# Optimization experiments

Hardware: AMD Instinct MI355X
Metric: run time of the kernel (lower is better)

Reference implementation:

```python
import jax, jax.numpy as jnp
import numpy as np

P = 384   # ssm_size
H = 768   # hidden_dim
K = 4     # conv_kernel
BATCH, LEN = 16, 2048


def setup_inputs() -> dict:
    key = jax.random.key(0)
    ks = jax.random.split(key, 12)
    inputs = jax.random.normal(ks[0], (BATCH, LEN, H), jnp.float32)
    # encoder
    Wl = jax.random.normal(ks[1], (H, H), jnp.float32) / np.sqrt(H)
    bl = jnp.zeros((H,), jnp.float32)
    conv_w = jax.random.normal(ks[2], (H, 1, K), jnp.float32) / np.sqrt(K)  # depthwise
    conv_b = jnp.zeros((H,), jnp.float32)
    # selective heads (zero-init in torch; small random for a non-trivial baseline)
    Wr = jax.random.normal(ks[3], (P, H), jnp.float32) * 0.01
    Wth = jax.random.normal(ks[4], (P, H), jnp.float32) * 0.01
    Winj = jax.random.normal(ks[5], (P, H), jnp.float32) * 0.01
    # ring init: |lambda| in [0.9, 1.0], arg in (0, pi)
    u = jax.random.uniform(ks[6], (P,), jnp.float32)
    mags = jnp.sqrt(u * (1.0 ** 2 - 0.9 ** 2) + 0.9 ** 2)
    r_base = jnp.log(mags / (1.0 - mags))              # logit
    args = jax.random.uniform(ks[7], (P,), jnp.float32, minval=1e-3, maxval=np.pi - 1e-3)
    th_base = jnp.arctanh(args / np.pi)
    dt_base = jax.random.normal(ks[8], (P,), jnp.float32) * 0.5
    inj_logit = jnp.full((P,), 2.0, jnp.float32)
    b_std = 1.0 / np.sqrt(H)
    c_std = 1.0 / np.sqrt(P)
    Bp = jax.random.uniform(ks[9], (P, H, 2), jnp.float32, minval=-b_std, maxval=b_std)
    Cp = jax.random.uniform(ks[10], (H, P, 2), jnp.float32, minval=-c_std, maxval=c_std)
    D = jax.random.normal(ks[11], (H,), jnp.float32)
    return dict(inputs=inputs, Wl=Wl, bl=bl, conv_w=conv_w, conv_b=conv_b,
                Wr=Wr, Wth=Wth, Winj=Winj, r_base=r_base, th_base=th_base,
                dt_base=dt_base, inj_logit=inj_logit, Bp=Bp, Cp=Cp, D=D)


def reference(inputs, Wl, bl, conv_w, conv_b, Wr, Wth, Winj,
              r_base, th_base, dt_base, inj_logit, Bp, Cp, D):
    Bsz, L, Hd = inputs.shape
    k = conv_w.shape[-1]
    # --- encoder: linear -> silu -> causal depthwise conv -> silu ---
    feats = jax.nn.silu(inputs @ Wl.T + bl)                       # (B,L,H)
    fc = jnp.transpose(feats, (0, 2, 1))                          # (B,H,L)
    fc = jax.lax.conv_general_dilated(
        fc, conv_w, window_strides=(1,), padding=[(k - 1, 0)],
        dimension_numbers=('NCH', 'OIH', 'NCH'), feature_group_count=Hd)
    feats = jnp.transpose(jax.nn.silu(fc + conv_b[None, :, None]), (0, 2, 1))  # (B,L,H)
    # --- spectral params ---
    r = jax.nn.sigmoid(r_base + feats @ Wr.T)                     # (B,L,P)
    theta = jnp.pi * jnp.tanh(th_base + feats @ Wth.T)            # (B,L,P)
    dt_floor = 0.02
    raw_dt = jax.nn.sigmoid(dt_base)                              # (P,) per_step_dt=False
    dt = jnp.broadcast_to(dt_floor + (1.0 - dt_floor) * raw_dt, r.shape)
    r2 = jnp.maximum(r * r, 1e-8)
    dtc = jnp.maximum(dt, 1e-6)
    cos_t = jnp.cos(theta)
    # imex1 variant
    A = (r2 - 2.0 * r * cos_t + 1.0) / (dtc * dtc * r2)
    G = (1.0 - r2) / (dtc * r2)
    # --- input projection (complex) + selective injection gate ---
    Bc = Bp[..., 0] + 1j * Bp[..., 1]                             # (P,H) complex64
    Cc = Cp[..., 0] + 1j * Cp[..., 1]                             # (H,P)
    bu = inputs.astype(jnp.complex64) @ Bc.T                      # (B,L,P)
    gate = jax.nn.sigmoid(inj_logit + feats @ Winj.T)
    bu = bu * gate
    # --- D-LinOSS IMEX1 scan over time ---
    A_s = jnp.transpose(A, (1, 0, 2))                             # (L,B,P)
    G_s = jnp.transpose(G, (1, 0, 2))
    dt_s = jnp.transpose(dtc, (1, 0, 2))
    bu_s = jnp.transpose(bu, (1, 0, 2))
    z0 = jnp.zeros((Bsz, A.shape[-1]), jnp.complex64)

    def step(carry, t):
        z, x = carry
        At, Gt, dtt, but = t
        S = 1.0 / (1.0 + dtt * Gt)          # implicit damping factor
        z = S * (z - (dtt * At) * x) + (S * dtt) * but
        x = x + dtt * z
        return (z, x), x

    _, xs = jax.lax.scan(step, (z0, z0), (A_s, G_s, dt_s, bu_s))  # (L,B,P)
    states = jnp.transpose(xs, (1, 0, 2))                         # (B,L,P)
    proj = jnp.real(states @ Cc.T)                                # (B,L,H)
    return proj + inputs * D
```

## Files before the change

kernel.cpp:

```cpp
#include <hip/hip_runtime.h>
#include <math.h>

#define PP 384
#define HH 768
#define KK 4
#define BB 16
#define LL 2048
#define MM (BB*LL)
#define NCH (BB*PP)
#define NC 32
#define CLEN (LL/NC)

typedef __attribute__((ext_vector_type(8))) short bf16x8;
typedef __attribute__((ext_vector_type(4))) float f32x4;

__device__ __forceinline__ float sigmoid_fast(float x) { return 1.0f / (1.0f + __expf(-x)); }

__device__ __forceinline__ float bf2f(unsigned short h) {
    return __uint_as_float(((unsigned int)h) << 16);
}
__device__ __forceinline__ unsigned short f2bf(float x) {
    unsigned int u = __float_as_uint(x);
    u += 0x7fff + ((u >> 16) & 1);
    return (unsigned short)(u >> 16);
}
__device__ __forceinline__ void split_bf(float x, unsigned short& hi, unsigned short& lo) {
    hi = f2bf(x);
    lo = f2bf(x - bf2f(hi));
}

__device__ __forceinline__ void gll16(const void* g, void* l) {
    __builtin_amdgcn_global_load_lds(
        (const __attribute__((address_space(1))) void*)g,
        (__attribute__((address_space(3))) void*)l, 16, 0, 0);
}

__device__ __forceinline__ void xcd_swizzle(int& bx, int& by) {
    const int gx = (int)gridDim.x;
    const int nwg = gx * (int)gridDim.y;
    const int orig = by * gx + bx;
    const int q = nwg >> 3, r = nwg & 7;
    const int xcd = orig & 7, off = orig >> 3;
    const int swz = (xcd < r ? xcd * (q + 1) : r * (q + 1) + (xcd - r) * q) + off;
    bx = swz % gx;
    by = swz / gx;
}

__device__ __forceinline__ void step_coef(float Rp, float Tp, float Ip,
    float rb, float tb, float il, float dt,
    float& c0, float& c1, float& gdt)
{
    const float PIf = 3.14159265358979323846f;
    float r  = sigmoid_fast(rb + Rp);
    float t  = tb + Tp;
    float e2 = __expf(2.0f * fabsf(t));
    float th = PIf * copysignf(1.0f - 2.0f / (e2 + 1.0f), t);
    float ct = __cosf(th);
    float r2 = fmaxf(r * r, 1e-8f);
    float Ac = (r2 - 2.0f * r * ct + 1.0f) / (dt * dt * r2);
    float Gc = (1.0f - r2) / (dt * r2);
    float S  = 1.0f / (1.0f + dt * Gc);
    float gate = sigmoid_fast(il + Ip);
    c0 = S;
    c1 = S * (dt * Ac);
    gdt = S * dt * gate;
}

__global__ __launch_bounds__(256) void repack_kernel(
    const float* __restrict__ Wl, const float* __restrict__ Wr,
    const float* __restrict__ Wth, const float* __restrict__ Winj,
    const float* __restrict__ Bp, const float* __restrict__ Cp,
    unsigned short* __restrict__ wlh, unsigned short* __restrict__ wll,
    unsigned short* __restrict__ wrth_h, unsigned short* __restrict__ wrth_l,
    unsigned short* __restrict__ winj,
    unsigned short* __restrict__ wb, unsigned short* __restrict__ wc)
{
    int i = blockIdx.x * 256 + threadIdx.x;
    const int NB = 768 * 768, NI = 384 * 768;
    if (i < NB) { split_bf(Wl[i], wlh[i], wll[i]); return; }
    i -= NB;
    if (i < NB) {
        int n = i / 768, k = i - n * 768;
        float v = (n < 384) ? Wr[n * 768 + k] : Wth[(n - 384) * 768 + k];
        split_bf(v, wrth_h[i], wrth_l[i]);
        return;
    }
    i -= NB;
    if (i < NI) { winj[i] = f2bf(Winj[i]); return; }
    i -= NI;
    if (i < NB) {
        int n = i / 768, k = i - n * 768;
        wb[i] = f2bf((n < 384) ? Bp[n * 1536 + k * 2] : Bp[(n - 384) * 1536 + k * 2 + 1]);
        return;
    }
    i -= NB;
    if (i < NB) {
        int n = i / 768, k = i - n * 768;
        wc[i] = f2bf((k < 384) ? Cp[n * 768 + k * 2] : -Cp[n * 768 + (k - 384) * 2 + 1]);
    }
}

__global__ __launch_bounds__(256) void split_convert_kernel(
    const float* __restrict__ in, unsigned short* __restrict__ outh,
    unsigned short* __restrict__ outl, int n4)
{
    int i = blockIdx.x * 256 + threadIdx.x;
    if (i >= n4) return;
    float4 a = ((const float4*)in)[i];
    ushort4 h, l;
    split_bf(a.x, h.x, l.x); split_bf(a.y, h.y, l.y);
    split_bf(a.z, h.z, l.z); split_bf(a.w, h.w, l.w);
    ((ushort4*)outh)[i] = h;
    ((ushort4*)outl)[i] = l;
}

template <int SMODE>
__global__ __launch_bounds__(256) void mfma_gemm_split(
    const unsigned short* __restrict__ Ah, const unsigned short* __restrict__ Al,
    const unsigned short* __restrict__ Wh, const unsigned short* __restrict__ Wl,
    float* __restrict__ Cout, int N, const float* __restrict__ bias)
{
    constexpr int K = 768;
    __shared__ unsigned short lsAh[128 * 32];
    __shared__ unsigned short lsAl[128 * 32];
    __shared__ unsigned short lsBh[128 * 32];
    __shared__ unsigned short lsBl[128 * 32];
    const int tid  = threadIdx.x;
    const int wave = tid >> 6, lane = tid & 63;
    const int wm = wave >> 1, wn = wave & 1;
    int bx = blockIdx.x, by = blockIdx.y;
    xcd_swizzle(bx, by);
    const int row0 = by * 128, col0 = bx * 128;

    const int srow = (wave << 4) + (lane >> 2);
    const int scol = (lane & 3) << 3;
    const size_t ga0 = (size_t)(row0 + srow) * K + scol;
    const size_t ga1 = (size_t)(row0 + 64 + srow) * K + scol;
    const size_t gb0 = (size_t)(col0 + srow) * K + scol;
    const size_t gb1 = (size_t)(col0 + 64 + srow) * K + scol;
    const int l0 = srow * 32 + scol;
    const int l1 = (64 + srow) * 32 + scol;

    f32x4 acc[4][4];
#pragma unroll
    for (int i = 0; i < 4; ++i)
#pragma unroll
        for (int j = 0; j < 4; ++j) acc[i][j] = (f32x4){0.f, 0.f, 0.f, 0.f};

    const int rfo = ((lane & 15) * 32) + ((lane >> 4) << 3);

    for (int kt = 0; kt < K; kt += 32) {
        __syncthreads();
        gll16(Ah + ga0 + kt, &lsAh[l0]);
        gll16(Ah + ga1 + kt, &lsAh[l1]);
        gll16(Al + ga0 + kt, &lsAl[l0]);
        gll16(Al + ga1 + kt, &lsAl[l1]);
        gll16(Wh + gb0 + kt, &lsBh[l0]);
        gll16(Wh + gb1 + kt, &lsBh[l1]);
        gll16(Wl + gb0 + kt, &lsBl[l0]);
        gll16(Wl + gb1 + kt, &lsBl[l1]);
        __syncthreads();
        bf16x8 afh[4], afl[4], bfh[4], bfl[4];
#pragma unroll
        for (int i = 0; i < 4; ++i) {
            afh[i] = *(const bf16x8*)&lsAh[(wm * 64 + i * 16) * 32 + rfo];
            afl[i] = *(const bf16x8*)&lsAl[(wm * 64 + i * 16) * 32 + rfo];
        }
#pragma unroll
        for (int j = 0; j < 4; ++j) {
            bfh[j] = *(const bf16x8*)&lsBh[(wn * 64 + j * 16) * 32 + rfo];
            bfl[j] = *(const bf16x8*)&lsBl[(wn * 64 + j * 16) * 32 + rfo];
        }
#pragma unroll
        for (int i = 0; i < 4; ++i)
#pragma unroll
            for (int j = 0; j < 4; ++j) {
                acc[i][j] = __builtin_amdgcn_mfma_f32_16x16x32_bf16(afh[i], bfh[j], acc[i][j], 0, 0, 0);
                acc[i][j] = __builtin_amdgcn_mfma_f32_16x16x32_bf16(afh[i], bfl[j], acc[i][j], 0, 0, 0);
                acc[i][j] = __builtin_amdgcn_mfma_f32_16x16x32_bf16(afl[i], bfh[j], acc[i][j], 0, 0, 0);
            }
    }

    const int rbase = row0 + wm * 64 + ((lane >> 4) << 2);
    const int cbase = col0 + wn * 64 + (lane & 15);
#pragma unroll
    for (int i = 0; i < 4; ++i) {
#pragma unroll
        for (int j = 0; j < 4; ++j) {
            const int cg = cbase + j * 16;
            float bv = (SMODE == 1) ? bias[cg] : 0.f;
#pragma unroll
            for (int q = 0; q < 4; ++q) {
                const int rg = rbase + i * 16 + q;
                const size_t off = (size_t)rg * N + cg;
                float v = acc[i][j][q];
                if (SMODE == 1) {
                    float x = v + bv;
                    Cout[off] = x * sigmoid_fast(x);
                } else {
                    Cout[off] = v;
                }
            }
        }
    }
}

template <int MODE>
__global__ __launch_bounds__(256) void mfma_gemm(
    const unsigned short* __restrict__ A, const unsigned short* __restrict__ W,
    void* __restrict__ Cout, int N,
    const float* __restrict__ resid, const float* __restrict__ Dv)
{
    constexpr int K = 768;
    __shared__ unsigned short lsA[128 * 32];
    __shared__ unsigned short lsB[128 * 32];
    const int tid  = threadIdx.x;
    const int wave = tid >> 6, lane = tid & 63;
    const int wm = wave >> 1, wn = wave & 1;
    int bx = blockIdx.x, by = blockIdx.y;
    xcd_swizzle(bx, by);
    const int row0 = by * 128, col0 = bx * 128;

    const int srow = (wave << 4) + (lane >> 2);
    const int scol = (lane & 3) << 3;
    const size_t ga0 = (size_t)(row0 + srow) * K + scol;
    const size_t ga1 = (size_t)(row0 + 64 + srow) * K + scol;
    const size_t gb0 = (size_t)(col0 + srow) * K + scol;
    const size_t gb1 = (size_t)(col0 + 64 + srow) * K + scol;
    const int l0 = srow * 32 + scol;
    const int l1 = (64 + srow) * 32 + scol;

    f32x4 acc[4][4];
#pragma unroll
    for (int i = 0; i < 4; ++i)
#pragma unroll
        for (int j = 0; j < 4; ++j) acc[i][j] = (f32x4){0.f, 0.f, 0.f, 0.f};

    const int rfo = ((lane & 15) * 32) + ((lane >> 4) << 3);

    for (int kt = 0; kt < K; kt += 32) {
        __syncthreads();
        gll16(A + ga0 + kt, &lsA[l0]);
        gll16(A + ga1 + kt, &lsA[l1]);
        gll16(W + gb0 + kt, &lsB[l0]);
        gll16(W + gb1 + kt, &lsB[l1]);
        __syncthreads();
        bf16x8 af[4], bfg[4];
#pragma unroll
        for (int i = 0; i < 4; ++i)
            af[i] = *(const bf16x8*)&lsA[(wm * 64 + i * 16) * 32 + rfo];
#pragma unroll
        for (int j = 0; j < 4; ++j)
            bfg[j] = *(const bf16x8*)&lsB[(wn * 64 + j * 16) * 32 + rfo];
#pragma unroll
        for (int i = 0; i < 4; ++i)
#pragma unroll
            for (int j = 0; j < 4; ++j)
                acc[i][j] = __builtin_amdgcn_mfma_f32_16x16x32_bf16(af[i], bfg[j], acc[i][j], 0, 0, 0);
    }

    const int rbase = row0 + wm * 64 + ((lane >> 4) << 2);
    const int cbase = col0 + wn * 64 + (lane & 15);
#pragma unroll
    for (int i = 0; i < 4; ++i) {
#pragma unroll
        for (int j = 0; j < 4; ++j) {
            const int cg = cbase + j * 16;
            float dv = (MODE == 2) ? Dv[cg] : 0.f;
#pragma unroll
            for (int q = 0; q < 4; ++q) {
                const int rg = rbase + i * 16 + q;
                const size_t off = (size_t)rg * N + cg;
                float v = acc[i][j][q];
                if (MODE == 2) {
                    ((float*)Cout)[off] = v + resid[off] * dv;
                } else {
                    ((unsigned short*)Cout)[off] = f2bf(v);
                }
            }
        }
    }
}

__global__ __launch_bounds__(256) void conv_silu_kernel(
    const float* __restrict__ x, const float* __restrict__ w,
    const float* __restrict__ cb, unsigned short* __restrict__ yh,
    unsigned short* __restrict__ yl)
{
    int idx = blockIdx.x * 256 + threadIdx.x;
    if (idx >= MM * HH) return;
    int h  = idx % HH;
    int ml = idx / HH;
    int l  = ml % LL;
    float acc = cb[h];
#pragma unroll
    for (int j = 0; j < KK; ++j) {
        int d = (KK - 1) - j;
        if (l - d >= 0) acc = fmaf(x[(size_t)(ml - d) * HH + h], w[h * KK + j], acc);
    }
    float y = acc * sigmoid_fast(acc);
    split_bf(y, yh[idx], yl[idx]);
}

__global__ __launch_bounds__(256) void scan_chunk_kernel(
    const float* __restrict__ heads_rt, const unsigned short* __restrict__ heads_inj,
    const unsigned short* __restrict__ bu,
    const float* __restrict__ r_base, const float* __restrict__ th_base,
    const float* __restrict__ dt_base, const float* __restrict__ inj,
    float4* __restrict__ summA, float4* __restrict__ summB)
{
    int g = blockIdx.x * 256 + threadIdx.x;
    if (g >= NC * NCH) return;
    int t = g % NCH;
    int j = g / NCH;
    int b = t / PP, p = t - b * PP;
    const float rb = r_base[p], tb = th_base[p], il = inj[p];
    const float dt = 0.02f + 0.98f * sigmoid_fast(dt_base[p]);
    float m00 = 1.f, m01 = 0.f, m10 = 0.f, m11 = 1.f;
    float vzR = 0.f, vxR = 0.f, vzI = 0.f, vxI = 0.f;
    const int mbase = b * LL + j * CLEN;
    for (int l = 0; l < CLEN; ++l) {
        const size_t m = (size_t)(mbase + l);
        const float Rp = heads_rt[m * 768 + p];
        const float Tp = heads_rt[m * 768 + 384 + p];
        const float Ip = bf2f(heads_inj[m * 384 + p]);
        const float b0 = bf2f(bu[m * 768 + p]);
        const float b1 = bf2f(bu[m * 768 + 384 + p]);
        float c0, c1, gdt;
        step_coef(Rp, Tp, Ip, rb, tb, il, dt, c0, c1, gdt);
        const float azR = gdt * b0, azI = gdt * b1;
        float nm00 = c0 * m00 - c1 * m10;
        float nm01 = c0 * m01 - c1 * m11;
        m10 = fmaf(dt, nm00, m10);
        m11 = fmaf(dt, nm01, m11);
        m00 = nm00; m01 = nm01;
        float nvzR = c0 * vzR - c1 * vxR + azR;
        vxR = fmaf(dt, nvzR, vxR); vzR = nvzR;
        float nvzI = c0 * vzI - c1 * vxI + azI;
        vxI = fmaf(dt, nvzI, vxI); vzI = nvzI;
    }
    summA[g] = make_float4(m00, m01, m10, m11);
    summB[g] = make_float4(vzR, vxR, vzI, vxI);
}

__global__ __launch_bounds__(256) void scan_mid_kernel(
    const float4* __restrict__ summA, const float4* __restrict__ summB,
    float4* __restrict__ starts)
{
    int t = blockIdx.x * 256 + threadIdx.x;
    if (t >= NCH) return;
    float zR = 0.f, xR = 0.f, zI = 0.f, xI = 0.f;
    for (int j = 0; j < NC; ++j) {
        starts[j * NCH + t] = make_float4(zR, xR, zI, xI);
        float4 Mv = summA[j * NCH + t];
        float4 Vv = summB[j * NCH + t];
        float nzR = Mv.x * zR + Mv.y * xR + Vv.x;
        float nxR = Mv.z * zR + Mv.w * xR + Vv.y;
        float nzI = Mv.x * zI + Mv.y * xI + Vv.z;
        float nxI = Mv.z * zI + Mv.w * xI + Vv.w;
        zR = nzR; xR = nxR; zI = nzI; xI = nxI;
    }
}

__global__ __launch_bounds__(256) void scan_apply_kernel(
    const float* __restrict__ heads_rt, const unsigned short* __restrict__ heads_inj,
    const unsigned short* __restrict__ bu,
    const float* __restrict__ r_base, const float* __restrict__ th_base,
    const float* __restrict__ dt_base, const float* __restrict__ inj,
    const float4* __restrict__ starts, unsigned short* __restrict__ states)
{
    int g = blockIdx.x * 256 + threadIdx.x;
    if (g >= NC * NCH) return;
    int t = g % NCH;
    int j = g / NCH;
    int b = t / PP, p = t - b * PP;
    const float rb = r_base[p], tb = th_base[p], il = inj[p];
    const float dt = 0.02f + 0.98f * sigmoid_fast(dt_base[p]);
    float4 s0 = starts[j * NCH + t];
    float zR = s0.x, xR = s0.y, zI = s0.z, xI = s0.w;
    const int mbase = b * LL + j * CLEN;
    for (int l = 0; l < CLEN; ++l) {
        const size_t m = (size_t)(mbase + l);
        const float Rp = heads_rt[m * 768 + p];
        const float Tp = heads_rt[m * 768 + 384 + p];
        const float Ip = bf2f(heads_inj[m * 384 + p]);
        const float b0 = bf2f(bu[m * 768 + p]);
        const float b1 = bf2f(bu[m * 768 + 384 + p]);
        float c0, c1, gdt;
        step_coef(Rp, Tp, Ip, rb, tb, il, dt, c0, c1, gdt);
        zR = c0 * zR - c1 * xR + gdt * b0;
        xR = fmaf(dt, zR, xR);
        zI = c0 * zI - c1 * xI + gdt * b1;
        xI = fmaf(dt, zI, xI);
        states[m * 768 + p]       = f2bf(xR);
        states[m * 768 + 384 + p] = f2bf(xI);
    }
}

extern "C" void kernel_launch(void* const* d_in, const int* in_sizes, int n_in,
                              void* d_out, int out_size, void* d_ws, size_t ws_size,
                              hipStream_t stream)
{
    const float* inputs  = (const float*)d_in[0];
    const float* Wl      = (const float*)d_in[1];
    const float* bl      = (const float*)d_in[2];
    const float* conv_w  = (const float*)d_in[3];
    const float* conv_b  = (const float*)d_in[4];
    const float* Wr      = (const float*)d_in[5];
    const float* Wth     = (const float*)d_in[6];
    const float* Winj    = (const float*)d_in[7];
    const float* r_base  = (const float*)d_in[8];
    const float* th_base = (const float*)d_in[9];
    const float* dt_base = (const float*)d_in[10];
    const float* inj_l   = (const float*)d_in[11];
    const float* Bp      = (const float*)d_in[12];
    const float* Cp      = (const float*)d_in[13];
    const float* Dv      = (const float*)d_in[14];
    float* out = (float*)d_out;

    const size_t NB = 768 * 768, NI = 384 * 768, NMH = (size_t)MM * 768;
    unsigned short* wlh    = (unsigned short*)d_ws;
    unsigned short* wll    = wlh + NB;
    unsigned short* wrth_h = wll + NB;
    unsigned short* wrth_l = wrth_h + NB;
    unsigned short* winj   = wrth_l + NB;
    unsigned short* wb     = winj + NI;
    unsigned short* wc     = wb + NB;
    unsigned short* inh    = wc + NB;
    unsigned short* inl    = inh + NMH;
    unsigned short* f2h    = inl + NMH;
    unsigned short* f2l    = f2h + NMH;
    unsigned short* hinj   = f2l + NMH;
    float* f1       = (float*)(hinj + (size_t)MM * 384);
    float* heads_rt = f1;
    float4* summA = (float4*)(f1 + NMH);
    float4* summB = summA + (size_t)NC * NCH;
    float4* starts= summB + (size_t)NC * NCH;
    unsigned short* bu = (unsigned short*)d_out;
    unsigned short* states = inl;

    {
        int total = (int)(4 * NB + NI);
        repack_kernel<<<(total + 255) / 256, 256, 0, stream>>>(
            Wl, Wr, Wth, Winj, Bp, Cp, wlh, wll, wrth_h, wrth_l, winj, wb, wc);
        int n4 = (int)(NMH / 4);
        split_convert_kernel<<<(n4 + 255) / 256, 256, 0, stream>>>(inputs, inh, inl, n4);
    }
    mfma_gemm_split<1><<<dim3(768 / 128, MM / 128), 256, 0, stream>>>(
        inh, inl, wlh, wll, f1, 768, bl);
    conv_silu_kernel<<<(MM * HH + 255) / 256, 256, 0, stream>>>(f1, conv_w, conv_b, f2h, f2l);
    mfma_gemm_split<0><<<dim3(768 / 128, MM / 128), 256, 0, stream>>>(
        f2h, f2l, wrth_h, wrth_l, heads_rt, 768, nullptr);
    mfma_gemm<3><<<dim3(384 / 128, MM / 128), 256, 0, stream>>>(
        f2h, winj, (void*)hinj, 384, nullptr, nullptr);
    mfma_gemm<3><<<dim3(768 / 128, MM / 128), 256, 0, stream>>>(
        inh, wb, (void*)bu, 768, nullptr, nullptr);
    scan_chunk_kernel<<<(NC * NCH) / 256, 256, 0, stream>>>(
        heads_rt, hinj, bu, r_base, th_base, dt_base, inj_l, summA, summB);
    scan_mid_kernel<<<(NCH + 255) / 256, 256, 0, stream>>>(summA, summB, starts);
    scan_apply_kernel<<<(NC * NCH) / 256, 256, 0, stream>>>(
        heads_rt, hinj, bu, r_base, th_base, dt_base, inj_l, starts, states);
    mfma_gemm<2><<<dim3(768 / 128, MM / 128), 256, 0, stream>>>(
        states, wc, (void*)out, 768, inputs, Dv);
}
```

Baseline: 720.0 us.

## Fuse GEMMs sharing an A operand, interleave complex layouts, vectorize conv and scan

The encoder GEMM and the bu projection now run as one launch with a wider grid, since both read the same input activations. The heads GEMM and the injection-gate GEMM are merged the same way. Blocks pick split-precision or plain bf16 paths by column range. Weight repacking interleaves real/imag and R/theta columns so the scan kernels use float2/ushort2 loads and stores. The depthwise conv is vectorized by 4 channels. The output GEMM now reads the bf16 high part of the inputs as its D residual instead of fp32, which lowers precision slightly. The goal is fewer launches, better load balance and wider memory accesses.

Result: slower. 872.6 us (+21.2%).

```diff
diff --git a/kernel.cpp b/kernel.cpp
--- a/kernel.cpp
+++ b/kernel.cpp
@@ -81,7 +81,8 @@
     i -= NB;
     if (i < NB) {
         int n = i / 768, k = i - n * 768;
-        float v = (n < 384) ? Wr[n * 768 + k] : Wth[(n - 384) * 768 + k];
+        int p = n >> 1;
+        float v = (n & 1) ? Wth[p * 768 + k] : Wr[p * 768 + k];
         split_bf(v, wrth_h[i], wrth_l[i]);
         return;
     }
@@ -90,13 +91,12 @@
     i -= NI;
     if (i < NB) {
         int n = i / 768, k = i - n * 768;
-        wb[i] = f2bf((n < 384) ? Bp[n * 1536 + k * 2] : Bp[(n - 384) * 1536 + k * 2 + 1]);
+        wb[i] = f2bf(Bp[(size_t)(n >> 1) * 1536 + k * 2 + (n & 1)]);
         return;
     }
     i -= NB;
     if (i < NB) {
-        int n = i / 768, k = i - n * 768;
-        wc[i] = f2bf((k < 384) ? Cp[n * 768 + k * 2] : -Cp[n * 768 + (k - 384) * 2 + 1]);
+        wc[i] = f2bf((i & 1) ? -Cp[i] : Cp[i]);
     }
 }
 
@@ -114,13 +114,17 @@
     ((ushort4*)outl)[i] = l;
 }
 
-template <int SMODE>
-__global__ __launch_bounds__(256) void mfma_gemm_split(
+template <int KIND>
+__global__ __launch_bounds__(256) void mfma_gemm_fused(
     const unsigned short* __restrict__ Ah, const unsigned short* __restrict__ Al,
-    const unsigned short* __restrict__ Wh, const unsigned short* __restrict__ Wl,
-    float* __restrict__ Cout, int N, const float* __restrict__ bias)
+    const unsigned short* __restrict__ Wsh, const unsigned short* __restrict__ Wsl,
+    const unsigned short* __restrict__ Wp,
+    float* __restrict__ outS, unsigned short* __restrict__ outP,
+    const float* __restrict__ bias)
 {
     constexpr int K = 768;
+    constexpr int NSPLIT = 768;
+    constexpr int STRIDE_P = (KIND == 0) ? 768 : 384;
     __shared__ unsigned short lsAh[128 * 32];
     __shared__ unsigned short lsAl[128 * 32];
     __shared__ unsigned short lsBh[128 * 32];
@@ -131,15 +135,18 @@
     int bx = blockIdx.x, by = blockIdx.y;
     xcd_swizzle(bx, by);
     const int row0 = by * 128, col0 = bx * 128;
+    const bool is_split = (col0 < NSPLIT);
+    const int bcol0 = is_split ? col0 : col0 - NSPLIT;
 
     const int srow = (wave << 4) + (lane >> 2);
     const int scol = (lane & 3) << 3;
     const size_t ga0 = (size_t)(row0 + srow) * K + scol;
     const size_t ga1 = (size_t)(row0 + 64 + srow) * K + scol;
-    const size_t gb0 = (size_t)(col0 + srow) * K + scol;
-    const size_t gb1 = (size_t)(col0 + 64 + srow) * K + scol;
+    const size_t gb0 = (size_t)(bcol0 + srow) * K + scol;
+    const size_t gb1 = (size_t)(bcol0 + 64 + srow) * K + scol;
     const int l0 = srow * 32 + scol;
     const int l1 = (64 + srow) * 32 + scol;
+    const unsigned short* Bh_src = is_split ? Wsh : Wp;
 
     f32x4 acc[4][4];
 #pragma unroll
@@ -153,32 +160,45 @@
         __syncthreads();
         gll16(Ah + ga0 + kt, &lsAh[l0]);
         gll16(Ah + ga1 + kt, &lsAh[l1]);
-        gll16(Al + ga0 + kt, &lsAl[l0]);
-        gll16(Al + ga1 + kt, &lsAl[l1]);
-        gll16(Wh + gb0 + kt, &lsBh[l0]);
-        gll16(Wh + gb1 + kt, &lsBh[l1]);
-        gll16(Wl + gb0 + kt, &lsBl[l0]);
-        gll16(Wl + gb1 + kt, &lsBl[l1]);
+        gll16(Bh_src + gb0 + kt, &lsBh[l0]);
+        gll16(Bh_src + gb1 + kt, &lsBh[l1]);
+        if (is_split) {
+            gll16(Al + ga0 + kt, &lsAl[l0]);
+            gll16(Al + ga1 + kt, &lsAl[l1]);
+            gll16(Wsl + gb0 + kt, &lsBl[l0]);
+            gll16(Wsl + gb1 + kt, &lsBl[l1]);
+        }
         __syncthreads();
-        bf16x8 afh[4], afl[4], bfh[4], bfl[4];
-#pragma unroll
-        for (int i = 0; i < 4; ++i) {
+        bf16x8 afh[4], bfh[4];
+#pragma unroll
+        for (int i = 0; i < 4; ++i)
             afh[i] = *(const bf16x8*)&lsAh[(wm * 64 + i * 16) * 32 + rfo];
-            afl[i] = *(const bf16x8*)&lsAl[(wm * 64 + i * 16) * 32 + rfo];
+#pragma unroll
+        for (int j = 0; j < 4; ++j)
+            bfh[j] = *(const bf16x8*)&lsBh[(wn * 64 + j * 16) * 32 + rfo];
+        if (is_split) {
+            bf16x8 afl[4], bfl[4];
+#pragma unroll
+            for (int i = 0; i < 4; ++i)
+                afl[i] = *(const bf16x8*)&lsAl[(wm * 64 + i * 16) * 32 + rfo];
+#pragma unroll
+            for (int j = 0; j < 4; ++j)
+                bfl[j] = *(const bf16x8*)&lsBl[(wn * 64 + j * 16) * 32 + rfo];
+#pragma unroll
+            for (int i = 0; i < 4; ++i)
+#pragma unroll
+                for (int j = 0; j < 4; ++j) {
+                    acc[i][j] = __builtin_amdgcn_mfma_f32_16x16x32_bf16(afh[i], bfh[j], acc[i][j], 0, 0, 0);
+                    acc[i][j] = __builtin_amdgcn_mfma_f32_16x16x32_bf16(afh[i], bfl[j], acc[i][j], 0, 0, 0);
+                    acc[i][j] = __builtin_amdgcn_mfma_f32_16x16x32_bf16(afl[i], bfh[j], acc[i][j], 0, 0, 0);
+                }
+        } else {
+#pragma unroll
+            for (int i = 0; i < 4; ++i)
+#pragma unroll
+                for (int j = 0; j < 4; ++j)
+                    acc[i][j] = __builtin_amdgcn_mfma_f32_16x16x32_bf16(afh[i], bfh[j], acc[i][j], 0, 0, 0);
         }
-#pragma unroll
-        for (int j = 0; j < 4; ++j) {
-            bfh[j] = *(const bf16x8*)&lsBh[(wn * 64 + j * 16) * 32 + rfo];
-            bfl[j] = *(const bf16x8*)&lsBl[(wn * 64 + j * 16) * 32 + rfo];
-        }
-#pragma unroll
-        for (int i = 0; i < 4; ++i)
-#pragma unroll
-            for (int j = 0; j < 4; ++j) {
-                acc[i][j] = __builtin_amdgcn_mfma_f32_16x16x32_bf16(afh[i], bfh[j], acc[i][j], 0, 0, 0);
-                acc[i][j] = __builtin_amdgcn_mfma_f32_16x16x32_bf16(afh[i], bfl[j], acc[i][j], 0, 0, 0);
-                acc[i][j] = __builtin_amdgcn_mfma_f32_16x16x32_bf16(afl[i], bfh[j], acc[i][j], 0, 0, 0);
-            }
     }
 
     const int rbase = row0 + wm * 64 + ((lane >> 4) << 2);
@@ -188,28 +208,32 @@
 #pragma unroll
         for (int j = 0; j < 4; ++j) {
             const int cg = cbase + j * 16;
-            float bv = (SMODE == 1) ? bias[cg] : 0.f;
+            float bv = (KIND == 0 && bias) ? bias[cg < NSPLIT ? cg : 0] : 0.f;
 #pragma unroll
             for (int q = 0; q < 4; ++q) {
                 const int rg = rbase + i * 16 + q;
-                const size_t off = (size_t)rg * N + cg;
                 float v = acc[i][j][q];
-                if (SMODE == 1) {
-                    float x = v + bv;
-                    Cout[off] = x * sigmoid_fast(x);
+                if (is_split) {
+                    const size_t off = (size_t)rg * 768 + cg;
+                    if (KIND == 0) {
+                        float x = v + bv;
+                        outS[off] = x * sigmoid_fast(x);
+                    } else {
+                        outS[off] = v;
+                    }
                 } else {
-                    Cout[off] = v;
+                    const size_t off = (size_t)rg * STRIDE_P + (cg - NSPLIT);
+                    outP[off] = f2bf(v);
                 }
             }
         }
     }
 }
 
-template <int MODE>
-__global__ __launch_bounds__(256) void mfma_gemm(
+__global__ __launch_bounds__(256) void mfma_gemm_out(
     const unsigned short* __restrict__ A, const unsigned short* __restrict__ W,
-    void* __restrict__ Cout, int N,
-    const float* __restrict__ resid, const float* __restrict__ Dv)
+    float* __restrict__ Cout, int N,
+    const unsigned short* __restrict__ resid, const float* __restrict__ Dv)
 {
     constexpr int K = 768;
     __shared__ unsigned short lsA[128 * 32];
@@ -266,17 +290,12 @@
 #pragma unroll
         for (int j = 0; j < 4; ++j) {
             const int cg = cbase + j * 16;
-            float dv = (MODE == 2) ? Dv[cg] : 0.f;
+            const float dv = Dv[cg];
 #pragma unroll
             for (int q = 0; q < 4; ++q) {
                 const int rg = rbase + i * 16 + q;
                 const size_t off = (size_t)rg * N + cg;
-                float v = acc[i][j][q];
-                if (MODE == 2) {
-                    ((float*)Cout)[off] = v + resid[off] * dv;
-                } else {
-                    ((unsigned short*)Cout)[off] = f2bf(v);
-                }
+                Cout[off] = acc[i][j][q] + bf2f(resid[off]) * dv;
             }
         }
     }
@@ -287,19 +306,33 @@
     const float* __restrict__ cb, unsigned short* __restrict__ yh,
     unsigned short* __restrict__ yl)
 {
-    int idx = blockIdx.x * 256 + threadIdx.x;
-    if (idx >= MM * HH) return;
-    int h  = idx % HH;
-    int ml = idx / HH;
+    int i4 = blockIdx.x * 256 + threadIdx.x;
+    if (i4 >= MM * HH / 4) return;
+    const int HQ = HH / 4;
+    int h4 = (i4 % HQ) * 4;
+    int ml = i4 / HQ;
     int l  = ml % LL;
-    float acc = cb[h];
+    float a0 = cb[h4], a1 = cb[h4 + 1], a2 = cb[h4 + 2], a3 = cb[h4 + 3];
 #pragma unroll
     for (int j = 0; j < KK; ++j) {
         int d = (KK - 1) - j;
-        if (l - d >= 0) acc = fmaf(x[(size_t)(ml - d) * HH + h], w[h * KK + j], acc);
-    }
-    float y = acc * sigmoid_fast(acc);
-    split_bf(y, yh[idx], yl[idx]);
+        if (l - d >= 0) {
+            float4 xv = *(const float4*)(x + (size_t)(ml - d) * HH + h4);
+            a0 = fmaf(xv.x, w[(h4 + 0) * KK + j], a0);
+            a1 = fmaf(xv.y, w[(h4 + 1) * KK + j], a1);
+            a2 = fmaf(xv.z, w[(h4 + 2) * KK + j], a2);
+            a3 = fmaf(xv.w, w[(h4 + 3) * KK + j], a3);
+        }
+    }
+    float y0 = a0 * sigmoid_fast(a0);
+    float y1 = a1 * sigmoid_fast(a1);
+    float y2 = a2 * sigmoid_fast(a2);
+    float y3 = a3 * sigmoid_fast(a3);
+    ushort4 vh, vl;
+    split_bf(y0, vh.x, vl.x); split_bf(y1, vh.y, vl.y);
+    split_bf(y2, vh.z, vl.z); split_bf(y3, vh.w, vl.w);
+    *(ushort4*)(yh + (size_t)i4 * 4) = vh;
+    *(ushort4*)(yl + (size_t)i4 * 4) = vl;
 }
 
 __global__ __launch_bounds__(256) void scan_chunk_kernel(
@@ -321,13 +354,12 @@
     const int mbase = b * LL + j * CLEN;
     for (int l = 0; l < CLEN; ++l) {
         const size_t m = (size_t)(mbase + l);
-        const float Rp = heads_rt[m * 768 + p];
-        const float Tp = heads_rt[m * 768 + 384 + p];
+        const float2 rt = *(const float2*)(heads_rt + m * 768 + 2 * p);
         const float Ip = bf2f(heads_inj[m * 384 + p]);
-        const float b0 = bf2f(bu[m * 768 + p]);
-        const float b1 = bf2f(bu[m * 768 + 384 + p]);
+        const ushort2 bv = *(const ushort2*)(bu + m * 768 + 2 * p);
+        const float b0 = bf2f(bv.x), b1 = bf2f(bv.y);
         float c0, c1, gdt;
-        step_coef(Rp, Tp, Ip, rb, tb, il, dt, c0, c1, gdt);
+        step_coef(rt.x, rt.y, Ip, rb, tb, il, dt, c0, c1, gdt);
         const float azR = gdt * b0, azI = gdt * b1;
         float nm00 = c0 * m00 - c1 * m10;
         float nm01 = c0 * m01 - c1 * m11;
@@ -381,19 +413,20 @@
     const int mbase = b * LL + j * CLEN;
     for (int l = 0; l < CLEN; ++l) {
         const size_t m = (size_t)(mbase + l);
-        const float Rp = heads_rt[m * 768 + p];
-        const float Tp = heads_rt[m * 768 + 384 + p];
+        const float2 rt = *(const float2*)(heads_rt + m * 768 + 2 * p);
         const float Ip = bf2f(heads_inj[m * 384 + p]);
-        const float b0 = bf2f(bu[m * 768 + p]);
-        const float b1 = bf2f(bu[m * 768 + 384 + p]);
+        const ushort2 bv = *(const ushort2*)(bu + m * 768 + 2 * p);
+        const float b0 = bf2f(bv.x), b1 = bf2f(bv.y);
         float c0, c1, gdt;
-        step_coef(Rp, Tp, Ip, rb, tb, il, dt, c0, c1, gdt);
+        step_coef(rt.x, rt.y, Ip, rb, tb, il, dt, c0, c1, gdt);
         zR = c0 * zR - c1 * xR + gdt * b0;
         xR = fmaf(dt, zR, xR);
         zI = c0 * zI - c1 * xI + gdt * b1;
         xI = fmaf(dt, zI, xI);
-        states[m * 768 + p]       = f2bf(xR);
-        states[m * 768 + 384 + p] = f2bf(xI);
+        ushort2 sv;
+        sv.x = f2bf(xR);
+        sv.y = f2bf(xI);
+        *(ushort2*)(states + m * 768 + 2 * p) = sv;
     }
 }
 
@@ -446,20 +479,16 @@
         int n4 = (int)(NMH / 4);
         split_convert_kernel<<<(n4 + 255) / 256, 256, 0, stream>>>(inputs, inh, inl, n4);
     }
-    mfma_gemm_split<1><<<dim3(768 / 128, MM / 128), 256, 0, stream>>>(
-        inh, inl, wlh, wll, f1, 768, bl);
-    conv_silu_kernel<<<(MM * HH + 255) / 256, 256, 0, stream>>>(f1, conv_w, conv_b, f2h, f2l);
-    mfma_gemm_split<0><<<dim3(768 / 128, MM / 128), 256, 0, stream>>>(
-        f2h, f2l, wrth_h, wrth_l, heads_rt, 768, nullptr);
-    mfma_gemm<3><<<dim3(384 / 128, MM / 128), 256, 0, stream>>>(
-        f2h, winj, (void*)hinj, 384, nullptr, nullptr);
-    mfma_gemm<3><<<dim3(768 / 128, MM / 128), 256, 0, stream>>>(
-        inh, wb, (void*)bu, 768, nullptr, nullptr);
+    mfma_gemm_fused<0><<<dim3(12, MM / 128), 256, 0, stream>>>(
+        inh, inl, wlh, wll, wb, f1, bu, bl);
+    conv_silu_kernel<<<(MM * HH / 4 + 255) / 256, 256, 0, stream>>>(f1, conv_w, conv_b, f2h, f2l);
+    mfma_gemm_fused<1><<<dim3(9, MM / 128), 256, 0, stream>>>(
+        f2h, f2l, wrth_h, wrth_l, winj, heads_rt, hinj, nullptr);
     scan_chunk_kernel<<<(NC * NCH) / 256, 256, 0, stream>>>(
         heads_rt, hinj, bu, r_base, th_base, dt_base, inj_l, summA, summB);
     scan_mid_kernel<<<(NCH + 255) / 256, 256, 0, stream>>>(summA, summB, starts);
     scan_apply_kernel<<<(NC * NCH) / 256, 256, 0, stream>>>(
         heads_rt, hinj, bu, r_base, th_base, dt_base, inj_l, starts, states);
-    mfma_gemm<2><<<dim3(768 / 128, MM / 128), 256, 0, stream>>>(
-        states, wc, (void*)out, 768, inputs, Dv);
-}
+    mfma_gemm_out<<<dim3(6, MM / 128), 256, 0, stream>>>(
+        states, wc, out, 768, inh, Dv);
+}
```

## Interleave real/imag weight columns, vectorize conv and scan accesses, use bf16 residual

Applied to the files above, without the earlier changes.

Repacks the Wr/Wth, B and C weights so real and imaginary (or R and theta) columns sit next to each other. The scan kernels can then load each pair with one float2 or ushort2 access and store states as a pair. The conv+silu kernel is vectorized to process four channels per thread with float4 loads and ushort4 stores. The final GEMM now reads the residual from the bf16-high split of the inputs instead of the fp32 inputs, which cuts traffic but reduces the precision of the D*inputs term.

After: 773.0 us. +7.4%, slower.

```diff
diff --git a/kernel.cpp b/kernel.cpp
--- a/kernel.cpp
+++ b/kernel.cpp
@@ -81,7 +81,8 @@
     i -= NB;
     if (i < NB) {
         int n = i / 768, k = i - n * 768;
-        float v = (n < 384) ? Wr[n * 768 + k] : Wth[(n - 384) * 768 + k];
+        int p = n >> 1;
+        float v = (n & 1) ? Wth[p * 768 + k] : Wr[p * 768 + k];
         split_bf(v, wrth_h[i], wrth_l[i]);
         return;
     }
@@ -90,13 +91,12 @@
     i -= NI;
     if (i < NB) {
         int n = i / 768, k = i - n * 768;
-        wb[i] = f2bf((n < 384) ? Bp[n * 1536 + k * 2] : Bp[(n - 384) * 1536 + k * 2 + 1]);
+        wb[i] = f2bf(Bp[(size_t)(n >> 1) * 1536 + k * 2 + (n & 1)]);
         return;
     }
     i -= NB;
     if (i < NB) {
-        int n = i / 768, k = i - n * 768;
-        wc[i] = f2bf((k < 384) ? Cp[n * 768 + k * 2] : -Cp[n * 768 + (k - 384) * 2 + 1]);
+        wc[i] = f2bf((i & 1) ? -Cp[i] : Cp[i]);
     }
 }
 
@@ -209,7 +209,7 @@
 __global__ __launch_bounds__(256) void mfma_gemm(
     const unsigned short* __restrict__ A, const unsigned short* __restrict__ W,
     void* __restrict__ Cout, int N,
-    const float* __restrict__ resid, const float* __restrict__ Dv)
+    const unsigned short* __restrict__ resid, const float* __restrict__ Dv)
 {
     constexpr int K = 768;
     __shared__ unsigned short lsA[128 * 32];
@@ -266,14 +266,14 @@
 #pragma unroll
         for (int j = 0; j < 4; ++j) {
             const int cg = cbase + j * 16;
-            float dv = (MODE == 2) ? Dv[cg] : 0.f;
+            const float dv = (MODE == 2) ? Dv[cg] : 0.f;
 #pragma unroll
             for (int q = 0; q < 4; ++q) {
                 const int rg = rbase + i * 16 + q;
                 const size_t off = (size_t)rg * N + cg;
                 float v = acc[i][j][q];
                 if (MODE == 2) {
-                    ((float*)Cout)[off] = v + resid[off] * dv;
+                    ((float*)Cout)[off] = v + bf2f(resid[off]) * dv;
                 } else {
                     ((unsigned short*)Cout)[off] = f2bf(v);
                 }
@@ -287,19 +287,33 @@
     const float* __restrict__ cb, unsigned short* __restrict__ yh,
     unsigned short* __restrict__ yl)
 {
-    int idx = blockIdx.x * 256 + threadIdx.x;
-    if (idx >= MM * HH) return;
-    int h  = idx % HH;
-    int ml = idx / HH;
+    int i4 = blockIdx.x * 256 + threadIdx.x;
+    if (i4 >= MM * HH / 4) return;
+    const int HQ = HH / 4;
+    int h4 = (i4 % HQ) * 4;
+    int ml = i4 / HQ;
     int l  = ml % LL;
-    float acc = cb[h];
+    float a0 = cb[h4], a1 = cb[h4 + 1], a2 = cb[h4 + 2], a3 = cb[h4 + 3];
 #pragma unroll
     for (int j = 0; j < KK; ++j) {
         int d = (KK - 1) - j;
-        if (l - d >= 0) acc = fmaf(x[(size_t)(ml - d) * HH + h], w[h * KK + j], acc);
-    }
-    float y = acc * sigmoid_fast(acc);
-    split_bf(y, yh[idx], yl[idx]);
+        if (l - d >= 0) {
+            float4 xv = *(const float4*)(x + (size_t)(ml - d) * HH + h4);
+            a0 = fmaf(xv.x, w[(h4 + 0) * KK + j], a0);
+            a1 = fmaf(xv.y, w[(h4 + 1) * KK + j], a1);
+            a2 = fmaf(xv.z, w[(h4 + 2) * KK + j], a2);
+            a3 = fmaf(xv.w, w[(h4 + 3) * KK + j], a3);
+        }
+    }
+    float y0 = a0 * sigmoid_fast(a0);
+    float y1 = a1 * sigmoid_fast(a1);
+    float y2 = a2 * sigmoid_fast(a2);
+    float y3 = a3 * sigmoid_fast(a3);
+    ushort4 vh, vl;
+    split_bf(y0, vh.x, vl.x); split_bf(y1, vh.y, vl.y);
+    split_bf(y2, vh.z, vl.z); split_bf(y3, vh.w, vl.w);
+    *(ushort4*)(yh + (size_t)i4 * 4) = vh;
+    *(ushort4*)(yl + (size_t)i4 * 4) = vl;
 }
 
 __global__ __launch_bounds__(256) void scan_chunk_kernel(
@@ -321,13 +335,12 @@
     const int mbase = b * LL + j * CLEN;
     for (int l = 0; l < CLEN; ++l) {
         const size_t m = (size_t)(mbase + l);
-        const float Rp = heads_rt[m * 768 + p];
-        const float Tp = heads_rt[m * 768 + 384 + p];
+        const float2 rt = *(const float2*)(heads_rt + m * 768 + 2 * p);
         const float Ip = bf2f(heads_inj[m * 384 + p]);
-        const float b0 = bf2f(bu[m * 768 + p]);
-        const float b1 = bf2f(bu[m * 768 + 384 + p]);
+        const ushort2 bv = *(const ushort2*)(bu + m * 768 + 2 * p);
+        const float b0 = bf2f(bv.x), b1 = bf2f(bv.y);
         float c0, c1, gdt;
-        step_coef(Rp, Tp, Ip, rb, tb, il, dt, c0, c1, gdt);
+        step_coef(rt.x, rt.y, Ip, rb, tb, il, dt, c0, c1, gdt);
         const float azR = gdt * b0, azI = gdt * b1;
         float nm00 = c0 * m00 - c1 * m10;
         float nm01 = c0 * m01 - c1 * m11;
@@ -381,19 +394,20 @@
     const int mbase = b * LL + j * CLEN;
     for (int l = 0; l < CLEN; ++l) {
         const size_t m = (size_t)(mbase + l);
-        const float Rp = heads_rt[m * 768 + p];
-        const float Tp = heads_rt[m * 768 + 384 + p];
+        const float2 rt = *(const float2*)(heads_rt + m * 768 + 2 * p);
         const float Ip = bf2f(heads_inj[m * 384 + p]);
-        const float b0 = bf2f(bu[m * 768 + p]);
-        const float b1 = bf2f(bu[m * 768 + 384 + p]);
+        const ushort2 bv = *(const ushort2*)(bu + m * 768 + 2 * p);
+        const float b0 = bf2f(bv.x), b1 = bf2f(bv.y);
         float c0, c1, gdt;
-        step_coef(Rp, Tp, Ip, rb, tb, il, dt, c0, c1, gdt);
+        step_coef(rt.x, rt.y, Ip, rb, tb, il, dt, c0, c1, gdt);
         zR = c0 * zR - c1 * xR + gdt * b0;
         xR = fmaf(dt, zR, xR);
         zI = c0 * zI - c1 * xI + gdt * b1;
         xI = fmaf(dt, zI, xI);
-        states[m * 768 + p]       = f2bf(xR);
-        states[m * 768 + 384 + p] = f2bf(xI);
+        ushort2 sv;
+        sv.x = f2bf(xR);
+        sv.y = f2bf(xI);
+        *(ushort2*)(states + m * 768 + 2 * p) = sv;
     }
 }
 
@@ -446,20 +460,20 @@
         int n4 = (int)(NMH / 4);
         split_convert_kernel<<<(n4 + 255) / 256, 256, 0, stream>>>(inputs, inh, inl, n4);
     }
-    mfma_gemm_split<1><<<dim3(768 / 128, MM / 128), 256, 0, stream>>>(
+    mfma_gemm_split<1><<<dim3(6, MM / 128), 256, 0, stream>>>(
         inh, inl, wlh, wll, f1, 768, bl);
-    conv_silu_kernel<<<(MM * HH + 255) / 256, 256, 0, stream>>>(f1, conv_w, conv_b, f2h, f2l);
-    mfma_gemm_split<0><<<dim3(768 / 128, MM / 128), 256, 0, stream>>>(
+    conv_silu_kernel<<<(MM * HH / 4 + 255) / 256, 256, 0, stream>>>(f1, conv_w, conv_b, f2h, f2l);
+    mfma_gemm_split<0><<<dim3(6, MM / 128), 256, 0, stream>>>(
         f2h, f2l, wrth_h, wrth_l, heads_rt, 768, nullptr);
-    mfma_gemm<3><<<dim3(384 / 128, MM / 128), 256, 0, stream>>>(
+    mfma_gemm<3><<<dim3(3, MM / 128), 256, 0, stream>>>(
         f2h, winj, (void*)hinj, 384, nullptr, nullptr);
-    mfma_gemm<3><<<dim3(768 / 128, MM / 128), 256, 0, stream>>>(
+    mfma_gemm<3><<<dim3(6, MM / 128), 256, 0, stream>>>(
         inh, wb, (void*)bu, 768, nullptr, nullptr);
     scan_chunk_kernel<<<(NC * NCH) / 256, 256, 0, stream>>>(
         heads_rt, hinj, bu, r_base, th_base, dt_base, inj_l, summA, summB);
     scan_mid_kernel<<<(NCH + 255) / 256, 256, 0, stream>>>(summA, summB, starts);
     scan_apply_kernel<<<(NC * NCH) / 256, 256, 0, stream>>>(
         heads_rt, hinj, bu, r_base, th_base, dt_base, inj_l, starts, states);
-    mfma_gemm<2><<<dim3(768 / 128, MM / 128), 256, 0, stream>>>(
-        states, wc, (void*)out, 768, inputs, Dv);
-}
+    mfma_gemm<2><<<dim3(6, MM / 128), 256, 0, stream>>>(
+        states, wc, (void*)out, 768, inh, Dv);
+}
```
